# Kernel optimization log

Measured on AMD Instinct MI355X. Metric: run time of the kernel, lower is better.

## Reference

```python
import jax, jax.numpy as jnp
import numpy as np

B, N, C, H = 32, 129, 768, 12
HID = 4 * C
EPS = 1e-5
NEG = -65504.0


def _layer_norm(x, g, b):
    mu = jnp.mean(x, axis=-1, keepdims=True)
    var = jnp.mean((x - mu) ** 2, axis=-1, keepdims=True)
    return (x - mu) / jnp.sqrt(var + EPS) * g + b


def _attn(x, m, g, b, wqkv, wproj):
    # x: [B, Nn, C], m: [B, Nn, 1] binary float mask
    Bb, Nn, Cc = x.shape
    hd = Cc // H
    xm = _layer_norm(x, g, b) * m
    qkv = (xm @ wqkv).reshape(Bb, Nn, 3, H, hd)
    q, k, v = (jnp.swapaxes(qkv[:, :, i], 1, 2) for i in range(3))  # [B,H,Nn,hd]
    att = jnp.einsum('bhqd,bhkd->bhqk', q, k) * (hd ** -0.5)
    outer = (m @ jnp.swapaxes(m, -1, -2))[:, None]  # [B,1,Nn,Nn] mask outer product
    att = jnp.where(outer == 0.0, NEG, att)
    att = jax.nn.softmax(att, axis=-1) * m[:, None]  # zero masked query rows
    out = jnp.einsum('bhqk,bhkd->bhqd', att, v)
    out = jnp.swapaxes(out, 1, 2).reshape(Bb, Nn, Cc)
    return out @ wproj


def _mlp(x, m, g, b, w1, w2):
    xm = _layer_norm(x, g, b) * m
    return jax.nn.gelu(xm @ w1, approximate=False) @ w2


def setup_inputs() -> dict:
    key = jax.random.key(0)
    ks = jax.random.split(key, 10)
    std = 0.02
    return {
        'RGB': jax.random.normal(ks[0], (B, N, C), jnp.float32),
        'NIR': jax.random.normal(ks[1], (B, N, C), jnp.float32),
        'TIR': jax.random.normal(ks[2], (B, N, C), jnp.float32),
        'mask': (jax.random.uniform(ks[3], (B, N - 1, 1)) > 0.3).astype(jnp.float32),
        'label': jax.random.randint(ks[4], (B,), 0, 171),
        # stacked params for branches [R, N, T, concat]
        'ln_g1': jnp.ones((4, C), jnp.float32),
        'ln_b1': jnp.zeros((4, C), jnp.float32),
        'w_qkv': std * jax.random.normal(ks[5], (4, C, 3 * C), jnp.float32),
        'w_proj': std * jax.random.normal(ks[6], (4, C, C), jnp.float32),
        'ln_g2': jnp.ones((4, C), jnp.float32),
        'ln_b2': jnp.zeros((4, C), jnp.float32),
        'w_fc1': std * jax.random.normal(ks[7], (4, C, HID), jnp.float32),
        'w_fc2': std * jax.random.normal(ks[8], (4, HID, C), jnp.float32),
        'out_g': jnp.ones((C,), jnp.float32),
        'out_b': jnp.zeros((C,), jnp.float32),
    }


def reference(RGB, NIR, TIR, mask, label, ln_g1, ln_b1, w_qkv, w_proj,
              ln_g2, ln_b2, w_fc1, w_fc2, out_g, out_b):
    m = jnp.concatenate([jnp.ones((RGB.shape[0], 1, 1), RGB.dtype), mask], axis=1)  # [B,N,1]

    def branch(x, i, mm):
        x = x + _attn(x, mm, ln_g1[i], ln_b1[i], w_qkv[i], w_proj[i])
        x = x + _mlp(x, mm, ln_g2[i], ln_b2[i], w_fc1[i], w_fc2[i])
        return x

    RGB = branch(RGB, 0, m)
    NIR = branch(NIR, 1, m)
    TIR = branch(TIR, 2, m)
    x = jnp.concatenate([RGB, NIR, TIR], axis=1)  # [B, 3N, C]
    m3 = jnp.tile(m, (1, 3, 1))
    x = branch(x, 3, m3)
    x = _layer_norm(x, out_g, out_b) * m3
    return x
```

## Files before the change

kernel.cpp:

```cpp
#include <hip/hip_runtime.h>

typedef unsigned short u16;
typedef __attribute__((ext_vector_type(4))) float f32x4;
typedef __attribute__((ext_vector_type(8))) short s16x8;
typedef __attribute__((ext_vector_type(4))) short s16x4;
typedef __attribute__((ext_vector_type(4))) unsigned short u16x4;

#define HH 12
#define CC 768
#define AS1(p) ((const __attribute__((address_space(1))) void*)(p))
#define AS3(p) ((__attribute__((address_space(3))) void*)(p))

__device__ inline u16 f2bf(float x){
  unsigned u = __float_as_uint(x);
  u = (u + 0x7FFFu + ((u >> 16) & 1u)) >> 16;
  return (u16)u;
}

__device__ inline f32x4 mfma32(s16x8 a, s16x8 b, f32x4 c){
  return __builtin_amdgcn_mfma_f32_16x16x32_bf16(a, b, c, 0, 0, 0);
}
__device__ inline f32x4 mfma16(s16x4 a, s16x4 b, f32x4 c){
  return __builtin_amdgcn_mfma_f32_16x16x16bf16_1k(a, b, c, 0, 0, 0);
}

__global__ void wtrans(const float* __restrict__ W, u16* __restrict__ Wt, int K, int N){
  __shared__ float tile[32][33];
  int k0 = blockIdx.x*32, n0 = blockIdx.y*32;
  const float* Wz = W + (size_t)blockIdx.z*K*N;
  u16* Wtz = Wt + (size_t)blockIdx.z*K*N;
  int tx = threadIdx.x & 31, ty = threadIdx.x >> 5;
  #pragma unroll
  for(int r = ty; r < 32; r += 8)
    tile[r][tx] = Wz[(size_t)(k0+r)*N + n0 + tx];
  __syncthreads();
  #pragma unroll
  for(int r = ty; r < 32; r += 8)
    Wtz[(size_t)(n0+r)*K + k0 + tx] = f2bf(tile[tx][r]);
}

__global__ void initcat(const float* __restrict__ R, const float* __restrict__ Nr,
                        const float* __restrict__ T, float* __restrict__ xcat){
  int idx = blockIdx.x*256 + threadIdx.x;
  const int per = 32*129*768/4;
  if(idx >= per) return;
  int z = blockIdx.y;
  const float* src = z == 0 ? R : (z == 1 ? Nr : T);
  float4 v = ((const float4*)src)[idx];
  int e = idx*4;
  int row = e / 768, c = e - row*768;
  int bb2 = row / 129, nn = row - bb2*129;
  ((float4*)xcat)[((size_t)(bb2*387 + z*129 + nn)*768 + c)/4] = v;
}

__device__ inline float maskval(const float* m, int b, int n){
  return (n == 0) ? 1.0f : m[b*128 + n - 1];
}

template<int F32OUT>
__global__ __launch_bounds__(64) void ln_mask(
    const float* __restrict__ x,
    const float* __restrict__ gg, const float* __restrict__ bb, int zsG,
    const float* __restrict__ mask,
    void* __restrict__ out, size_t zsO,
    int tpb, int zoffmul)
{
  int r = blockIdx.x, z = blockIdx.y, lane = threadIdx.x;
  int bidx = r / tpb, nn = r - bidx*tpb;
  size_t cat = (size_t)bidx*387 + z*zoffmul + nn;
  const float4* xr = (const float4*)(x + cat*CC);
  float4 v[3]; float s = 0.f, sq = 0.f;
  #pragma unroll
  for(int w = 0; w < 3; ++w){
    v[w] = xr[w*64 + lane];
    s  += v[w].x + v[w].y + v[w].z + v[w].w;
    sq += v[w].x*v[w].x + v[w].y*v[w].y + v[w].z*v[w].z + v[w].w*v[w].w;
  }
  #pragma unroll
  for(int o = 32; o; o >>= 1){ s += __shfl_xor(s, o); sq += __shfl_xor(sq, o); }
  float mu = s * (1.f/768.f);
  float var = sq * (1.f/768.f) - mu*mu;
  float rstd = rsqrtf(var + 1e-5f);
  float mv = maskval(mask, bidx, nn % 129);
  const float4* g4 = (const float4*)(gg + (size_t)z*zsG);
  const float4* b4 = (const float4*)(bb + (size_t)z*zsG);
  #pragma unroll
  for(int w = 0; w < 3; ++w){
    float4 gv = g4[w*64+lane], bv = b4[w*64+lane];
    float y0 = ((v[w].x - mu)*rstd*gv.x + bv.x) * mv;
    float y1 = ((v[w].y - mu)*rstd*gv.y + bv.y) * mv;
    float y2 = ((v[w].z - mu)*rstd*gv.z + bv.z) * mv;
    float y3 = ((v[w].w - mu)*rstd*gv.w + bv.w) * mv;
    if(F32OUT){
      ((float4*)out)[cat*(CC/4) + w*64 + lane] = make_float4(y0,y1,y2,y3);
    } else {
      u16x4 p; p.x = f2bf(y0); p.y = f2bf(y1); p.z = f2bf(y2); p.w = f2bf(y3);
      ((u16x4*)((u16*)out + z*zsO + (size_t)r*CC))[w*64 + lane] = p;
    }
  }
}

template<int EPI, int TPB>
__global__ __launch_bounds__(256, 4) void gemm_bt(
    const u16* __restrict__ A, size_t zsA,
    const u16* __restrict__ Bt, size_t zsB,
    void* __restrict__ O, size_t zsO,
    int M, int N, int K,
    int zoffmul)
{
  __shared__ u16 As[128*64];
  __shared__ u16 Bs[128*64];
  int z = blockIdx.z;
  const u16* Az = A + zsA*(size_t)z;
  const u16* Bz = Bt + zsB*(size_t)z;

  int gx = gridDim.x, gy = gridDim.y;
  int nwg = gx*gy;
  int orig = blockIdx.x + gx*blockIdx.y;
  int q = nwg >> 3, r8 = nwg & 7;
  int xcd = orig & 7, off = orig >> 3;
  int wg = (xcd < r8 ? xcd*(q+1) : r8*(q+1) + (xcd-r8)*q) + off;
  int bx = wg / gy, by = wg - bx*gy;
  int m0 = bx*128, n0 = by*128;

  int tid = threadIdx.x, wid = tid >> 6, lane = tid & 63;
  int wr = wid >> 1, wc = wid & 1;
  int lrow = lane & 15, g4 = lane >> 4;

  int srow = tid >> 3;
  int swcol = ((tid & 7) ^ (srow & 7)) * 8;
  const u16 *pa[4], *pb[4];
  #pragma unroll
  for(int i = 0; i < 4; ++i){
    int ra = m0 + srow + i*32; ra = ra < M ? ra : M - 1;
    pa[i] = Az + (size_t)ra*K + swcol;
    pb[i] = Bz + (size_t)(n0 + srow + i*32)*K + swcol;
  }
  int dofs = tid*8;

  int xs0 = ((0*4 + g4) ^ (lrow & 7)) * 8;
  int xs1 = ((1*4 + g4) ^ (lrow & 7)) * 8;

  f32x4 acc[4][4] = {};
  int NT = K >> 6;

  for(int t = 0; t < NT; ++t){
    #pragma unroll
    for(int i = 0; i < 4; ++i)
      __builtin_amdgcn_global_load_lds(AS1(pa[i]), AS3(&As[dofs + i*2048]), 16, 0, 0);
    #pragma unroll
    for(int i = 0; i < 4; ++i)
      __builtin_amdgcn_global_load_lds(AS1(pb[i]), AS3(&Bs[dofs + i*2048]), 16, 0, 0);
    #pragma unroll
    for(int i = 0; i < 4; ++i){ pa[i] += 64; pb[i] += 64; }
    __syncthreads();
    #pragma unroll
    for(int kk = 0; kk < 2; ++kk){
      int xs = kk ? xs1 : xs0;
      s16x8 aF[4], bF[4];
      #pragma unroll
      for(int i = 0; i < 4; ++i){
        aF[i] = *(const s16x8*)&As[(wr*64 + i*16 + lrow)*64 + xs];
        bF[i] = *(const s16x8*)&Bs[(wc*64 + i*16 + lrow)*64 + xs];
      }
      #pragma unroll
      for(int i = 0; i < 4; ++i)
        #pragma unroll
        for(int jn = 0; jn < 4; ++jn)
          acc[i][jn] = mfma32(aF[i], bF[jn], acc[i][jn]);
    }
    __syncthreads();
  }

  u16* Oz = (u16*)O + zsO*(size_t)z;
  int zb = z*zoffmul;
  #pragma unroll
  for(int i = 0; i < 4; ++i){
    #pragma unroll
    for(int r = 0; r < 4; ++r){
      int row = m0 + wr*64 + i*16 + g4*4 + r;
      if(row >= M) continue;
      #pragma unroll
      for(int jn = 0; jn < 4; ++jn){
        int col = n0 + wc*64 + jn*16 + lrow;
        float v = acc[i][jn][r];
        if constexpr (EPI == 0){
          Oz[(size_t)row*N + col] = f2bf(v);
        } else if constexpr (EPI == 1){
          float u = v*(0.7978845608f + 0.0356774081f*v*v);
          float t = 1.f - 2.f/(__expf(2.f*u) + 1.f);
          Oz[(size_t)row*N + col] = f2bf(0.5f*v*(1.f + t));
        } else {
          int bi = row / TPB, nnn = row - bi*TPB;
          size_t cat = (size_t)bi*387 + zb + nnn;
          float* dst = (float*)O + cat*CC + col;
          *dst += v;
        }
      }
    }
  }
}

template<int N_>
__global__ __launch_bounds__(256) void attn3(
    const u16* __restrict__ qkv, size_t zsQ,
    u16* __restrict__ out, size_t zsO,
    const float* __restrict__ mask)
{
  constexpr int NC  = (N_ + 63)/64;
  constexpr int NKC = NC*64;
  constexpr float SCL = 0.125f*1.44269504088896f;
  __shared__ u16 Ks[2][64][66];
  __shared__ u16 Vt[2][64][68];
  __shared__ float Msk[NKC];

  int z = blockIdx.z;
  int bh = blockIdx.y, b = bh / HH, hh = bh - b*HH;
  int tid = threadIdx.x, wid = tid >> 6, lane = tid & 63;
  int lq = lane & 15, g = lane >> 4;
  const u16* qz = qkv + zsQ*(size_t)z;
  const size_t rowbase = (size_t)b*N_;
  const u16* kbase = qz + rowbase*2304 + 768 + hh*64;
  const u16* vbase = kbase + 768;

  for(int k = tid; k < NKC; k += 256){
    float mk = 0.f;
    if(k < N_){ int nn = (N_ > 129) ? (k % 129) : k; mk = (nn == 0) ? 1.f : mask[b*128 + nn - 1]; }
    Msk[k] = (mk != 0.f) ? 0.f : -1e30f;
  }

  int q0 = blockIdx.x*64 + wid*16;
  int qrow = q0 + lq;
  int qrc = qrow < N_ ? qrow : N_ - 1;
  const u16* qptr = qz + (rowbase + qrc)*2304 + hh*64;
  s16x8 qF0 = *(const s16x8*)(qptr + g*8);
  s16x8 qF1 = *(const s16x8*)(qptr + 32 + g*8);

  int r0 = tid >> 3, c16 = tid & 7;
  s16x8 kr[2], vr[2];
  const s16x8 zv = {0,0,0,0,0,0,0,0};

  #pragma unroll
  for(int i = 0; i < 2; ++i){
    int row = r0 + i*32;
    kr[i] = (row < N_) ? *(const s16x8*)(kbase + (size_t)row*2304 + c16*8) : zv;
    vr[i] = (row < N_) ? *(const s16x8*)(vbase + (size_t)row*2304 + c16*8) : zv;
  }
  #pragma unroll
  for(int i = 0; i < 2; ++i){
    *(s16x8*)&Ks[0][r0 + i*32][c16*8] = kr[i];
    #pragma unroll
    for(int j = 0; j < 8; ++j) Vt[0][c16*8 + j][r0 + i*32] = (u16)vr[i][j];
  }
  __syncthreads();

  f32x4 o[4] = {};
  float l = 0.f;

  for(int ch = 0; ch < NC; ++ch){
    int cur = ch & 1;
    if(ch + 1 < NC){
      #pragma unroll
      for(int i = 0; i < 2; ++i){
        int row = (ch + 1)*64 + r0 + i*32;
        kr[i] = (row < N_) ? *(const s16x8*)(kbase + (size_t)row*2304 + c16*8) : zv;
        vr[i] = (row < N_) ? *(const s16x8*)(vbase + (size_t)row*2304 + c16*8) : zv;
      }
    }
    float pT[4][4];
    #pragma unroll
    for(int t = 0; t < 4; ++t){
      s16x8 kF0 = *(const s16x8*)&Ks[cur][t*16 + lq][g*8];
      s16x8 kF1 = *(const s16x8*)&Ks[cur][t*16 + lq][32 + g*8];
      f32x4 s = {0.f,0.f,0.f,0.f};
      s = mfma32(kF0, qF0, s);
      s = mfma32(kF1, qF1, s);
      const float* mrow = &Msk[ch*64 + t*16 + g*4];
      #pragma unroll
      for(int r = 0; r < 4; ++r){
        float p = exp2f(fmaf(s[r], SCL, mrow[r]));
        pT[t][r] = p;
        l += p;
      }
    }
    #pragma unroll
    for(int t = 0; t < 4; ++t){
      s16x4 pa;
      #pragma unroll
      for(int r = 0; r < 4; ++r) pa[r] = (short)f2bf(pT[t][r]);
      #pragma unroll
      for(int db = 0; db < 4; ++db){
        s16x4 vf = *(const s16x4*)&Vt[cur][db*16 + lq][t*16 + g*4];
        o[db] = mfma16(pa, vf, o[db]);
      }
    }
    if(ch + 1 < NC){
      int nxt = (ch + 1) & 1;
      #pragma unroll
      for(int i = 0; i < 2; ++i){
        *(s16x8*)&Ks[nxt][r0 + i*32][c16*8] = kr[i];
        #pragma unroll
        for(int j = 0; j < 8; ++j) Vt[nxt][c16*8 + j][r0 + i*32] = (u16)vr[i][j];
      }
      __syncthreads();
    }
  }

  l += __shfl_xor(l, 16);
  l += __shfl_xor(l, 32);
  float mq = 0.f;
  if(qrow < N_) mq = (Msk[qrow] == 0.f) ? 1.f : 0.f;
  float sc = mq / l;
  float scr[4];
  #pragma unroll
  for(int r = 0; r < 4; ++r) scr[r] = __shfl(sc, g*4 + r);

  #pragma unroll
  for(int db = 0; db < 4; ++db){
    #pragma unroll
    for(int r = 0; r < 4; ++r){
      int qq = q0 + g*4 + r;
      if(qq < N_)
        out[zsO*(size_t)z + (rowbase + qq)*CC + hh*64 + db*16 + lq] = f2bf(o[db][r]*scr[r]);
    }
  }
}

extern "C" void kernel_launch(void* const* d_in, const int* in_sizes, int n_in,
                              void* d_out, int out_size, void* d_ws, size_t ws_size,
                              hipStream_t stream)
{
  const float* RGB   = (const float*)d_in[0];
  const float* NIR   = (const float*)d_in[1];
  const float* TIR   = (const float*)d_in[2];
  const float* mask  = (const float*)d_in[3];
  const float* ln_g1 = (const float*)d_in[5];
  const float* ln_b1 = (const float*)d_in[6];
  const float* w_qkv = (const float*)d_in[7];
  const float* w_proj= (const float*)d_in[8];
  const float* ln_g2 = (const float*)d_in[9];
  const float* ln_b2 = (const float*)d_in[10];
  const float* w_fc1 = (const float*)d_in[11];
  const float* w_fc2 = (const float*)d_in[12];
  const float* out_g = (const float*)d_in[13];
  const float* out_b = (const float*)d_in[14];

  char* p = (char*)d_ws;
  u16* wqkv_t  = (u16*)p; p += (size_t)4*2304*768*2;
  u16* wproj_t = (u16*)p; p += (size_t)4*768*768*2;
  u16* w1_t    = (u16*)p; p += (size_t)4*768*3072*2;
  u16* w2_t    = (u16*)p; p += (size_t)4*3072*768*2;
  float* xcat  = (float*)p; p += (size_t)12384*768*4;
  u16* xm      = (u16*)p; p += (size_t)3*4224*768*2;
  u16* qkv     = (u16*)p; p += (size_t)3*4224*3072*2;
  u16* hbuf    = qkv;
  if((size_t)(p - (char*)d_ws) > ws_size) return;

  wtrans<<<dim3(24, 72, 4), 256, 0, stream>>>(w_qkv, wqkv_t, 768, 2304);
  wtrans<<<dim3(24, 24, 4), 256, 0, stream>>>(w_proj, wproj_t, 768, 768);
  wtrans<<<dim3(24, 96, 4), 256, 0, stream>>>(w_fc1, w1_t, 768, 3072);
  wtrans<<<dim3(96, 24, 4), 256, 0, stream>>>(w_fc2, w2_t, 3072, 768);
  initcat<<<dim3(3096, 3), 256, 0, stream>>>(RGB, NIR, TIR, xcat);

  const int M3 = 4128;
  const size_t zxm = (size_t)4224*768, zqkv = (size_t)4224*2304, zh = (size_t)4224*3072;
  ln_mask<0><<<dim3(M3,3), 64, 0, stream>>>(xcat, ln_g1, ln_b1, 768, mask, xm, zxm, 129, 129);
  gemm_bt<0,1><<<dim3(33,18,3), 256, 0, stream>>>(xm, zxm, wqkv_t, (size_t)2304*768, qkv, zqkv, M3, 2304, 768, 0);
  attn3<129><<<dim3(3,384,3), 256, 0, stream>>>(qkv, zqkv, xm, zxm, mask);
  gemm_bt<2,129><<<dim3(33,6,3), 256, 0, stream>>>(xm, zxm, wproj_t, (size_t)768*768, xcat, 0, M3, 768, 768, 129);
  ln_mask<0><<<dim3(M3,3), 64, 0, stream>>>(xcat, ln_g2, ln_b2, 768, mask, xm, zxm, 129, 129);
  gemm_bt<1,1><<<dim3(33,24,3), 256, 0, stream>>>(xm, zxm, w1_t, (size_t)768*3072, hbuf, zh, M3, 3072, 768, 0);
  gemm_bt<2,129><<<dim3(33,6,3), 256, 0, stream>>>(hbuf, zh, w2_t, (size_t)768*3072, xcat, 0, M3, 768, 3072, 129);
  const int M1 = 12384;
  ln_mask<0><<<dim3(M1,1), 64, 0, stream>>>(xcat, ln_g1 + 3*768, ln_b1 + 3*768, 0, mask, xm, 0, 387, 0);
  gemm_bt<0,1><<<dim3(97,18,1), 256, 0, stream>>>(xm, 0, wqkv_t + (size_t)3*2304*768, 0, qkv, 0, M1, 2304, 768, 0);
  attn3<387><<<dim3(7,384,1), 256, 0, stream>>>(qkv, 0, xm, 0, mask);
  gemm_bt<2,387><<<dim3(97,6,1), 256, 0, stream>>>(xm, 0, wproj_t + (size_t)3*768*768, 0, xcat, 0, M1, 768, 768, 0);
  ln_mask<0><<<dim3(M1,1), 64, 0, stream>>>(xcat, ln_g2 + 3*768, ln_b2 + 3*768, 0, mask, xm, 0, 387, 0);
  gemm_bt<1,1><<<dim3(97,24,1), 256, 0, stream>>>(xm, 0, w1_t + (size_t)3*768*3072, 0, hbuf, 0, M1, 3072, 768, 0);
  gemm_bt<2,387><<<dim3(97,6,1), 256, 0, stream>>>(hbuf, 0, w2_t + (size_t)3*768*3072, 0, xcat, 0, M1, 768, 3072, 0);
  ln_mask<1><<<dim3(M1,1), 64, 0, stream>>>(xcat, out_g, out_b, 0, mask, d_out, 0, 387, 0);
}
```

Measured before the change: 709.7 us.

## Add 256x256 eight-wave double-buffered GEMM for QKV and MLP projections

Introduces a new GEMM kernel with 256x256 output tiles, 512 threads and double-buffered LDS. The next K-slice is prefetched in four staged chunks interleaved with MFMA quarter-tiles, with wave priority raised around the MFMA bursts. It replaces the 128x128 kernel for the QKV, fc1 and fc2 GEMMs, aiming at higher data reuse per LDS load and overlap of global-to-LDS loads with compute. The cost is far fewer workgroups (fc2 drops to about 150 blocks), one block per CU, and more padding waste on M.

```diff
diff --git a/kernel.cpp b/kernel.cpp
--- a/kernel.cpp
+++ b/kernel.cpp
@@ -22,6 +22,19 @@
 }
 __device__ inline f32x4 mfma16(s16x4 a, s16x4 b, f32x4 c){
   return __builtin_amdgcn_mfma_f32_16x16x16bf16_1k(a, b, c, 0, 0, 0);
+}
+
+__device__ inline void xcd_remap(int gx, int gy, int& bx, int& by){
+  int nwg = gx*gy;
+  int orig = blockIdx.x + gx*blockIdx.y;
+  int q = nwg >> 3, r8 = nwg & 7;
+  int xcd = orig & 7, off = orig >> 3;
+  int wg = (xcd < r8 ? xcd*(q+1) : r8*(q+1) + (xcd-r8)*q) + off;
+  bx = wg / gy; by = wg - bx*gy;
+}
+
+__device__ inline void epi_store(float v, int row, int col, void* O, size_t zsO,
+                                 int z, int N, int zoffmul, int EPI, int TPB){
 }
 
 __global__ void wtrans(const float* __restrict__ W, u16* __restrict__ Wt, int K, int N){
@@ -113,14 +126,7 @@
   int z = blockIdx.z;
   const u16* Az = A + zsA*(size_t)z;
   const u16* Bz = Bt + zsB*(size_t)z;
-
-  int gx = gridDim.x, gy = gridDim.y;
-  int nwg = gx*gy;
-  int orig = blockIdx.x + gx*blockIdx.y;
-  int q = nwg >> 3, r8 = nwg & 7;
-  int xcd = orig & 7, off = orig >> 3;
-  int wg = (xcd < r8 ? xcd*(q+1) : r8*(q+1) + (xcd-r8)*q) + off;
-  int bx = wg / gy, by = wg - bx*gy;
+  int bx, by; xcd_remap(gridDim.x, gridDim.y, bx, by);
   int m0 = bx*128, n0 = by*128;
 
   int tid = threadIdx.x, wid = tid >> 6, lane = tid & 63;
@@ -137,7 +143,6 @@
     pb[i] = Bz + (size_t)(n0 + srow + i*32)*K + swcol;
   }
   int dofs = tid*8;
-
   int xs0 = ((0*4 + g4) ^ (lrow & 7)) * 8;
   int xs1 = ((1*4 + g4) ^ (lrow & 7)) * 8;
 
@@ -184,6 +189,178 @@
       for(int jn = 0; jn < 4; ++jn){
         int col = n0 + wc*64 + jn*16 + lrow;
         float v = acc[i][jn][r];
+        if constexpr (EPI == 0){
+          Oz[(size_t)row*N + col] = f2bf(v);
+        } else if constexpr (EPI == 1){
+          float u = v*(0.7978845608f + 0.0356774081f*v*v);
+          float t = 1.f - 2.f/(__expf(2.f*u) + 1.f);
+          Oz[(size_t)row*N + col] = f2bf(0.5f*v*(1.f + t));
+        } else {
+          int bi = row / TPB, nnn = row - bi*TPB;
+          size_t cat = (size_t)bi*387 + zb + nnn;
+          float* dst = (float*)O + cat*CC + col;
+          *dst += v;
+        }
+      }
+    }
+  }
+}
+
+template<int EPI, int TPB>
+__global__ __launch_bounds__(512, 1) void gemm8(
+    const u16* __restrict__ A, size_t zsA,
+    const u16* __restrict__ Bt, size_t zsB,
+    void* __restrict__ O, size_t zsO,
+    int M, int N, int K,
+    int zoffmul)
+{
+  __shared__ u16 As[2][256*64];
+  __shared__ u16 Bs[2][256*64];
+  int z = blockIdx.z;
+  const u16* Az = A + zsA*(size_t)z;
+  const u16* Bz = Bt + zsB*(size_t)z;
+  int bx, by; xcd_remap(gridDim.x, gridDim.y, bx, by);
+  int m0 = bx*256, n0 = by*256;
+
+  int tid = threadIdx.x, wid = tid >> 6, lane = tid & 63;
+  int wr = wid >> 2, wc = wid & 3;
+  int lrow = lane & 15, g4 = lane >> 4;
+
+  int srow = tid >> 3;
+  int swcol = ((tid & 7) ^ (srow & 7)) * 8;
+  const u16 *pa[4], *pb[4];
+  #pragma unroll
+  for(int i = 0; i < 4; ++i){
+    int ra = m0 + srow + i*64; ra = ra < M ? ra : M - 1;
+    pa[i] = Az + (size_t)ra*K + swcol;
+    pb[i] = Bz + (size_t)(n0 + srow + i*64)*K + swcol;
+  }
+  int dofs = tid*8;
+
+  int xsk[2];
+  xsk[0] = ((0*4 + g4) ^ (lrow & 7)) * 8;
+  xsk[1] = ((1*4 + g4) ^ (lrow & 7)) * 8;
+
+  #pragma unroll
+  for(int i = 0; i < 4; ++i)
+    __builtin_amdgcn_global_load_lds(AS1(pa[i]), AS3(&As[0][dofs + i*4096]), 16, 0, 0);
+  #pragma unroll
+  for(int i = 0; i < 4; ++i)
+    __builtin_amdgcn_global_load_lds(AS1(pb[i]), AS3(&Bs[0][dofs + i*4096]), 16, 0, 0);
+  #pragma unroll
+  for(int i = 0; i < 4; ++i){ pa[i] += 64; pb[i] += 64; }
+
+  f32x4 acc[8][4] = {};
+  int NT = K >> 6;
+
+  for(int t = 0; t < NT; ++t){
+    int cur = t & 1, nx = cur ^ 1;
+    bool pf = (t + 1 < NT);
+    s16x8 aF[4][2], bL[2][2], bH[2][2];
+
+    if(pf){
+      #pragma unroll
+      for(int i = 0; i < 2; ++i)
+        __builtin_amdgcn_global_load_lds(AS1(pa[i]), AS3(&As[nx][dofs + i*4096]), 16, 0, 0);
+      asm volatile("s_waitcnt vmcnt(2)" ::: "memory");
+    } else {
+      asm volatile("s_waitcnt vmcnt(0)" ::: "memory");
+    }
+    asm volatile("s_barrier" ::: "memory");
+    #pragma unroll
+    for(int mi = 0; mi < 4; ++mi)
+      #pragma unroll
+      for(int ks = 0; ks < 2; ++ks)
+        aF[mi][ks] = *(const s16x8*)&As[cur][(wr*128 + mi*16 + lrow)*64 + xsk[ks]];
+    #pragma unroll
+    for(int ni = 0; ni < 2; ++ni)
+      #pragma unroll
+      for(int ks = 0; ks < 2; ++ks)
+        bL[ni][ks] = *(const s16x8*)&Bs[cur][(wc*64 + ni*16 + lrow)*64 + xsk[ks]];
+    __builtin_amdgcn_s_setprio(1);
+    #pragma unroll
+    for(int mi = 0; mi < 4; ++mi)
+      #pragma unroll
+      for(int ni = 0; ni < 2; ++ni)
+        #pragma unroll
+        for(int ks = 0; ks < 2; ++ks)
+          acc[mi][ni] = mfma32(aF[mi][ks], bL[ni][ks], acc[mi][ni]);
+    __builtin_amdgcn_s_setprio(0);
+    asm volatile("s_barrier" ::: "memory");
+
+    #pragma unroll
+    for(int ni = 0; ni < 2; ++ni)
+      #pragma unroll
+      for(int ks = 0; ks < 2; ++ks)
+        bH[ni][ks] = *(const s16x8*)&Bs[cur][(wc*64 + (2+ni)*16 + lrow)*64 + xsk[ks]];
+    if(pf){
+      #pragma unroll
+      for(int i = 2; i < 4; ++i)
+        __builtin_amdgcn_global_load_lds(AS1(pa[i]), AS3(&As[nx][dofs + i*4096]), 16, 0, 0);
+    }
+    __builtin_amdgcn_s_setprio(1);
+    #pragma unroll
+    for(int mi = 0; mi < 4; ++mi)
+      #pragma unroll
+      for(int ni = 0; ni < 2; ++ni)
+        #pragma unroll
+        for(int ks = 0; ks < 2; ++ks)
+          acc[mi][2+ni] = mfma32(aF[mi][ks], bH[ni][ks], acc[mi][2+ni]);
+    __builtin_amdgcn_s_setprio(0);
+    asm volatile("s_barrier" ::: "memory");
+
+    #pragma unroll
+    for(int mi = 0; mi < 4; ++mi)
+      #pragma unroll
+      for(int ks = 0; ks < 2; ++ks)
+        aF[mi][ks] = *(const s16x8*)&As[cur][(wr*128 + (4+mi)*16 + lrow)*64 + xsk[ks]];
+    if(pf){
+      #pragma unroll
+      for(int i = 0; i < 2; ++i)
+        __builtin_amdgcn_global_load_lds(AS1(pb[i]), AS3(&Bs[nx][dofs + i*4096]), 16, 0, 0);
+    }
+    __builtin_amdgcn_s_setprio(1);
+    #pragma unroll
+    for(int mi = 0; mi < 4; ++mi)
+      #pragma unroll
+      for(int ni = 0; ni < 2; ++ni)
+        #pragma unroll
+        for(int ks = 0; ks < 2; ++ks)
+          acc[4+mi][2+ni] = mfma32(aF[mi][ks], bH[ni][ks], acc[4+mi][2+ni]);
+    __builtin_amdgcn_s_setprio(0);
+    asm volatile("s_barrier" ::: "memory");
+
+    if(pf){
+      #pragma unroll
+      for(int i = 2; i < 4; ++i)
+        __builtin_amdgcn_global_load_lds(AS1(pb[i]), AS3(&Bs[nx][dofs + i*4096]), 16, 0, 0);
+      #pragma unroll
+      for(int i = 0; i < 4; ++i){ pa[i] += 64; pb[i] += 64; }
+    }
+    __builtin_amdgcn_s_setprio(1);
+    #pragma unroll
+    for(int mi = 0; mi < 4; ++mi)
+      #pragma unroll
+      for(int ni = 0; ni < 2; ++ni)
+        #pragma unroll
+        for(int ks = 0; ks < 2; ++ks)
+          acc[4+mi][ni] = mfma32(aF[mi][ks], bL[ni][ks], acc[4+mi][ni]);
+    __builtin_amdgcn_s_setprio(0);
+    asm volatile("s_barrier" ::: "memory");
+  }
+
+  u16* Oz = (u16*)O + zsO*(size_t)z;
+  int zb = z*zoffmul;
+  #pragma unroll
+  for(int mi = 0; mi < 8; ++mi){
+    #pragma unroll
+    for(int r = 0; r < 4; ++r){
+      int row = m0 + wr*128 + mi*16 + g4*4 + r;
+      if(row >= M) continue;
+      #pragma unroll
+      for(int ni = 0; ni < 4; ++ni){
+        int col = n0 + wc*64 + ni*16 + lrow;
+        float v = acc[mi][ni][r];
         if constexpr (EPI == 0){
           Oz[(size_t)row*N + col] = f2bf(v);
         } else if constexpr (EPI == 1){
@@ -365,19 +542,19 @@
   const int M3 = 4128;
   const size_t zxm = (size_t)4224*768, zqkv = (size_t)4224*2304, zh = (size_t)4224*3072;
   ln_mask<0><<<dim3(M3,3), 64, 0, stream>>>(xcat, ln_g1, ln_b1, 768, mask, xm, zxm, 129, 129);
-  gemm_bt<0,1><<<dim3(33,18,3), 256, 0, stream>>>(xm, zxm, wqkv_t, (size_t)2304*768, qkv, zqkv, M3, 2304, 768, 0);
+  gemm8<0,1><<<dim3(17,9,3), 512, 0, stream>>>(xm, zxm, wqkv_t, (size_t)2304*768, qkv, zqkv, M3, 2304, 768, 0);
   attn3<129><<<dim3(3,384,3), 256, 0, stream>>>(qkv, zqkv, xm, zxm, mask);
   gemm_bt<2,129><<<dim3(33,6,3), 256, 0, stream>>>(xm, zxm, wproj_t, (size_t)768*768, xcat, 0, M3, 768, 768, 129);
   ln_mask<0><<<dim3(M3,3), 64, 0, stream>>>(xcat, ln_g2, ln_b2, 768, mask, xm, zxm, 129, 129);
-  gemm_bt<1,1><<<dim3(33,24,3), 256, 0, stream>>>(xm, zxm, w1_t, (size_t)768*3072, hbuf, zh, M3, 3072, 768, 0);
-  gemm_bt<2,129><<<dim3(33,6,3), 256, 0, stream>>>(hbuf, zh, w2_t, (size_t)768*3072, xcat, 0, M3, 768, 3072, 129);
+  gemm8<1,1><<<dim3(17,12,3), 512, 0, stream>>>(xm, zxm, w1_t, (size_t)768*3072, hbuf, zh, M3, 3072, 768, 0);
+  gemm8<2,129><<<dim3(17,3,3), 512, 0, stream>>>(hbuf, zh, w2_t, (size_t)768*3072, xcat, 0, M3, 768, 3072, 129);
   const int M1 = 12384;
   ln_mask<0><<<dim3(M1,1), 64, 0, stream>>>(xcat, ln_g1 + 3*768, ln_b1 + 3*768, 0, mask, xm, 0, 387, 0);
-  gemm_bt<0,1><<<dim3(97,18,1), 256, 0, stream>>>(xm, 0, wqkv_t + (size_t)3*2304*768, 0, qkv, 0, M1, 2304, 768, 0);
+  gemm8<0,1><<<dim3(49,9,1), 512, 0, stream>>>(xm, 0, wqkv_t + (size_t)3*2304*768, 0, qkv, 0, M1, 2304, 768, 0);
   attn3<387><<<dim3(7,384,1), 256, 0, stream>>>(qkv, 0, xm, 0, mask);
   gemm_bt<2,387><<<dim3(97,6,1), 256, 0, stream>>>(xm, 0, wproj_t + (size_t)3*768*768, 0, xcat, 0, M1, 768, 768, 0);
   ln_mask<0><<<dim3(M1,1), 64, 0, stream>>>(xcat, ln_g2 + 3*768, ln_b2 + 3*768, 0, mask, xm, 0, 387, 0);
-  gemm_bt<1,1><<<dim3(97,24,1), 256, 0, stream>>>(xm, 0, w1_t + (size_t)3*768*3072, 0, hbuf, 0, M1, 3072, 768, 0);
-  gemm_bt<2,387><<<dim3(97,6,1), 256, 0, stream>>>(hbuf, 0, w2_t + (size_t)3*768*3072, 0, xcat, 0, M1, 768, 3072, 0);
+  gemm8<1,1><<<dim3(49,12,1), 512, 0, stream>>>(xm, 0, w1_t + (size_t)3*768*3072, 0, hbuf, 0, M1, 3072, 768, 0);
+  gemm8<2,387><<<dim3(49,3,1), 512, 0, stream>>>(hbuf, 0, w2_t + (size_t)3*768*3072, 0, xcat, 0, M1, 768, 3072, 0);
   ln_mask<1><<<dim3(M1,1), 64, 0, stream>>>(xcat, out_g, out_b, 0, mask, d_out, 0, 387, 0);
 }
```

Result: slower. 818.6 us (+15.3%).
